# Performance work log

Measured on AMD Instinct MI355X. Metric: run time of the kernel, lower is better.

## Reference

```python
import jax, jax.numpy as jnp
import numpy as np

INP = 512
HIDDEN = 512
N_HEADS = 8          # called 'head_dim' in the torch code
D_HEAD = HIDDEN // N_HEADS  # 64
BASE = 10000.0
SCALE = D_HEAD ** (-0.5)


def rope(x):
    # x: [b, s, h, d]
    b, s, h, d = x.shape
    half = d // 2
    theta = 1.0 / (BASE ** (jnp.arange(0, d, 2, dtype=jnp.float32) / d))  # [d/2]
    idx_theta = jnp.arange(s, dtype=jnp.float32)[:, None] * theta[None, :]  # [s, d/2]
    idx_theta2 = jnp.concatenate([idx_theta, idx_theta], axis=1)            # [s, d]
    neg_half = jnp.concatenate([-x[..., half:], x[..., :half]], axis=-1)
    cos = jnp.cos(idx_theta2)[None, :, None, :]
    sin = jnp.sin(idx_theta2)[None, :, None, :]
    return x * cos + neg_half * sin


def setup_inputs() -> dict:
    key = jax.random.key(0)
    ks = jax.random.split(key, 10)
    b, s = 4, 2048
    init = lambda k, shp, fan_in: jax.random.normal(k, shp, jnp.float32) * (fan_in ** -0.5)
    return {
        "x": jax.random.normal(ks[0], (b, s, INP), jnp.float32),
        "c": jax.random.normal(ks[1], (b, s, INP), jnp.float32),
        "Wq": init(ks[2], (INP, HIDDEN), INP), "bq": jnp.zeros((HIDDEN,), jnp.float32),
        "Wk": init(ks[3], (INP, HIDDEN), INP), "bk": jnp.zeros((HIDDEN,), jnp.float32),
        "Wv": init(ks[4], (INP, HIDDEN), INP), "bv": jnp.zeros((HIDDEN,), jnp.float32),
        "Wo": init(ks[5], (HIDDEN, INP), HIDDEN), "bo": jnp.zeros((INP,), jnp.float32),
    }


def reference(x, c, Wq, bq, Wk, bk, Wv, bv, Wo, bo):
    b, s, _ = x.shape
    h_res = x
    q = (c @ Wq + bq).reshape(b, s, N_HEADS, D_HEAD)
    k = (x @ Wk + bk).reshape(b, s, N_HEADS, D_HEAD)
    v = (x @ Wv + bv).reshape(b, s, N_HEADS, D_HEAD)
    q = rope(q)
    k = rope(k)  # computed but unused, exactly as in the source
    # NOTE: source computes scores between q and V (not k) -- faithful reproduction
    att = jnp.einsum('bihd,bjhd->bhij', q, v)            # [b, h, s, s]
    att = jax.nn.softmax(att * SCALE, axis=-1)
    out = jnp.einsum('bhij,bjhd->bihd', att, v)          # [b, s, h, d]
    out = out.reshape(b, s, HIDDEN)
    out = out @ Wo + bo
    return out + h_res
```

## Files before the change

### kernel.cpp

```cpp
#include <hip/hip_runtime.h>
#include <hip/hip_bf16.h>
#include <cstdint>

typedef float f32x4 __attribute__((ext_vector_type(4)));
typedef float f32x16 __attribute__((ext_vector_type(16)));
typedef short bf16x8 __attribute__((ext_vector_type(8)));
typedef short bf16x4 __attribute__((ext_vector_type(4)));
typedef unsigned int u32x2 __attribute__((ext_vector_type(2)));
typedef unsigned short u16;

#define B_    4
#define S_    2048
#define H_    8
#define D_    64
#define M_    8192

#define OFF_CBF   0UL
#define OFF_XBF   8388608UL
#define OFF_QBH   16777216UL
#define OFF_VBH   25165824UL
#define OFF_VTBH  33554432UL
#define OFF_ATTN  41943040UL
#define OFF_WQT   50331648UL
#define OFF_WVT   50855936UL
// ... 12 lines not shown
    union { uint32_t u; float f; } v; v.u = ((uint32_t)h) << 16;
    return v.f;
}

__device__ __forceinline__ uint32_t cvtpk(float lo, float hi){
    uint32_t r;
    asm("v_cvt_pk_bf16_f32 %0, %1, %2" : "=v"(r) : "v"(lo), "v"(hi));
    return r;
}
__device__ __forceinline__ void plswap(uint32_t &va, uint32_t &vb){
#if __has_builtin(__builtin_amdgcn_permlane32_swap)
    u32x2 r = __builtin_amdgcn_permlane32_swap(va, vb, false, false);
    va = r[0]; vb = r[1];
#else
    asm volatile("v_permlane32_swap_b32 %0, %1" : "+v"(va), "+v"(vb));
#endif
}

__device__ __forceinline__ f32x16 mfma32(bf16x8 a, bf16x8 b, f32x16 c){
    return __builtin_amdgcn_mfma_f32_32x32x16_bf16(a, b, c, 0, 0, 0);
}

__device__ __forceinline__ void deint(uint4 a, uint4 b, bf16x8 &lo, bf16x8 &hi){
    union { bf16x8 v; uint32_t d[4]; } L, H;
    uint32_t s0=a.x, s1=a.y, s2=a.z, s3=a.w, s4=b.x, s5=b.y, s6=b.z, s7=b.w;
    L.d[0] = (s0 & 0xffffu) | (s1 << 16);
    L.d[1] = (s2 & 0xffffu) | (s3 << 16);
    L.d[2] = (s4 & 0xffffu) | (s5 << 16);
    L.d[3] = (s6 & 0xffffu) | (s7 << 16);
    H.d[0] = (s0 >> 16) | (s1 & 0xffff0000u);
    H.d[1] = (s2 >> 16) | (s3 & 0xffff0000u);
    H.d[2] = (s4 >> 16) | (s5 & 0xffff0000u);
    H.d[3] = (s6 >> 16) | (s7 & 0xffff0000u);
    lo = L.v; hi = H.v;
}

__device__ __forceinline__ int swz(int row, int col){
    return (col & ~63) | ((((col >> 3) & 7) ^ (row & 7)) << 3) | (col & 7);
}

__device__ __forceinline__ int detect_f32(const void* x_in){
    int lane = threadIdx.x & 63;
    ushort2 dv = ((const ushort2*)x_in)[lane];
    bool hit = ((((dv.x >> 7) & 0xFF) >= 160) || (((dv.y >> 7) & 0xFF) >= 160));
    return __ballot(hit) != 0ULL;
}

__device__ __forceinline__ void gload_lds16(const u16* g, u16* l){
    __builtin_amdgcn_global_load_lds(
        (const __attribute__((address_space(1))) void*)g,
        (__attribute__((address_space(3))) void*)l, 16, 0, 0);
}

__global__ void k_prep(const void* c_in, const void* x_in,
                       const void* Wq, const void* Wv, const void* Wo,
                       const void* bq, const void* bv, const void* bo,
                       u16* c_bf, u16* x_bf,
                       u16* Wqt, u16* Wvt, u16* Wot, float* bias_ws,
                       float* cos_t, float* sin_t){
    int bid = blockIdx.x;
    if (bid >= 11264){
        int idx = (bid - 11264) * 256 + threadIdx.x;
        int pos = idx >> 5, j = idx & 31;
        double theta = pow(10000.0, -(double)j / 32.0);
        double rev = ((double)pos * theta) * 0.15915494309189535;
        rev -= floor(rev);
        float fr = (float)rev;
        cos_t[idx] = __builtin_amdgcn_cosf(fr);
        sin_t[idx] = __builtin_amdgcn_sinf(fr);
        return;
    }
    if (bid >= 8192){
        int f = detect_f32(x_in);
        int wi = (bid - 8192) >> 10;
        int idx = ((bid - 8192) & 1023) * 256 + threadIdx.x;
        int k = idx >> 9, n = idx & 511;
        const void* W; u16* Wt; const void* bb;
        if (wi == 0){ W = Wq; Wt = Wqt; bb = bq; }
        else if (wi == 1){ W = Wv; Wt = Wvt; bb = bv; }
        else { W = Wo; Wt = Wot; bb = bo; }
        float v = f ? ((const float*)W)[idx] : bf2f(((const u16*)W)[idx]);
        Wt[n * 512 + (wi == 2 ? k : swz(n, k))] = f2bf(v);
        if (idx < 512){
            float b = f ? ((const float*)bb)[idx] : bf2f(((const u16*)bb)[idx]);
            bias_ws[wi * 512 + idx] = b;
        }
        return;
    }
    int f = detect_f32(x_in);
    int isx = bid >= 4096;
    int t = (bid & 4095) * 256 + threadIdx.x;
    const void* src = isx ? x_in : c_in;
    u16* dst = isx ? x_bf : c_bf;
    int e0 = t * 4, row = e0 >> 9, col = e0 & 511;
    size_t didx = (size_t)row * 512 + swz(row, col);
    ushort4 o;
    if (f){
        float4 v = ((const float4*)src)[t];
        o.x = f2bf(v.x); o.y = f2bf(v.y); o.z = f2bf(v.z); o.w = f2bf(v.w);
    } else {
        o = ((const ushort4*)src)[t];
    }
    *(ushort4*)(dst + didx) = o;
}

__global__ __launch_bounds__(256) void k_gemm_qv(
    const u16* __restrict__ c_bf, const u16* __restrict__ x_bf,
    const u16* __restrict__ Wqt, const u16* __restrict__ Wvt,
    const float* __restrict__ bias_ws,
    const float* __restrict__ cos_t, const float* __restrict__ sin_t,
    u16* __restrict__ Qbh, u16* __restrict__ Vbh, u16* __restrict__ Vtbh)
{
    __shared__ __align__(16) u16 Als[2][128 * 64];
    __shared__ __align__(16) u16 Bls[2][128 * 64];
    const int w = threadIdx.x >> 6, lane = threadIdx.x & 63;
    const int g = lane >> 4, cq = lane & 15;
    const int wm = w & 1, wn = w >> 1;
    const int z = blockIdx.z;
    const u16* A  = z ? x_bf : c_bf;
    const u16* Wt = z ? Wvt : Wqt;
    const float* bias = bias_ws + (z ? 512 : 0);
    const int m0b = blockIdx.x * 128, n0b = blockIdx.y * 128;
    const int m0 = m0b + wm * 64, n0 = n0b + wn * 64;
    const int swzi = ((cq & 7) << 3);

    int srow[4], scol[4];
    #pragma unroll
    for (int i = 0; i < 4; i++){
        int flat = (w * 4 + i) * 64 + lane;
        srow[i] = flat >> 3; scol[i] = (flat & 7) * 8;
    }

    const f32x4 zero = {0.f, 0.f, 0.f, 0.f};
    f32x4 acc[4][4];
    #pragma unroll
    for (int i = 0; i < 4; i++)
        #pragma unroll
        for (int j = 0; j < 4; j++) acc[i][j] = zero;

    #pragma unroll
    for (int i = 0; i < 4; i++){
        gload_lds16(A  + (size_t)(m0b + srow[i]) * 512 + scol[i], &Als[0][(w*4 + i) * 512]);
        gload_lds16(Wt + (size_t)(n0b + srow[i]) * 512 + scol[i], &Bls[0][(w*4 + i) * 512]);
    }

    for (int kt = 0; kt < 8; kt++){
        const int buf = kt & 1;
        __builtin_amdgcn_s_waitcnt(0x0F70);
        __syncthreads();
        if (kt < 7){
            const int kk = (kt + 1) * 64;
            #pragma unroll
            for (int i = 0; i < 4; i++){
                gload_lds16(A  + (size_t)(m0b + srow[i]) * 512 + kk + scol[i], &Als[buf^1][(w*4 + i) * 512]);
                gload_lds16(Wt + (size_t)(n0b + srow[i]) * 512 + kk + scol[i], &Bls[buf^1][(w*4 + i) * 512]);
            }
        }
        #pragma unroll
        for (int ks = 0; ks < 2; ks++){
            const int cs = ((ks * 4 + g) << 3) ^ swzi;
            bf16x8 a[4], b[4];
            #pragma unroll
            for (int mt = 0; mt < 4; mt++)
                a[mt] = *(const bf16x8*)&Als[buf][(wm*64 + mt*16 + cq) * 64 + cs];
            #pragma unroll
            for (int nt = 0; nt < 4; nt++)
                b[nt] = *(const bf16x8*)&Bls[buf][(wn*64 + nt*16 + cq) * 64 + cs];
            #pragma unroll
            for (int mt = 0; mt < 4; mt++)
                #pragma unroll
                for (int nt = 0; nt < 4; nt++)
                    acc[mt][nt] = __builtin_amdgcn_mfma_f32_16x16x32_bf16(a[mt], b[nt], acc[mt][nt], 0, 0, 0);
        }
    }
    __syncthreads();

    #pragma unroll
    for (int nt = 0; nt < 4; nt++){
        float bvv = bias[n0 + nt*16 + cq];
        #pragma unroll
        for (int mt = 0; mt < 4; mt++) acc[mt][nt] += bvv;
    }
    const int h = n0 >> 6;
    if (z == 0){
        const float SCL = 0.125f * 1.4426950408889634f;
        uint32_t* Qpk = (uint32_t*)Qbh;
        #pragma unroll
        for (int mt = 0; mt < 4; mt++){
            #pragma unroll
            for (int r = 0; r < 4; r++){
                int row = m0 + mt*16 + g*4 + r;
                int b_idx = row >> 11, si = row & 2047;
                size_t base = ((size_t)(b_idx*8 + h) * 2048 + si) * 32;
                #pragma unroll
                for (int nt = 0; nt < 2; nt++){
                    int dj = nt*16 + cq;
                    float cv = cos_t[si*32 + dj], sv = sin_t[si*32 + dj];
                    float x1 = acc[mt][nt][r], x2 = acc[mt][nt+2][r];
                    Qpk[base + dj] = cvtpk((x1*cv - x2*sv) * SCL, (x2*cv + x1*sv) * SCL);
                }
            }
        }
    } else {
        float* ltw = ((float*)&Als[0][0]) + w * (16 * 65);
        const int b_idx = m0 >> 11, si0 = m0 & 2047;
        const size_t tbase = ((size_t)(b_idx*8 + h) * 64) * 2048;
        #pragma unroll
        for (int mt = 0; mt < 4; mt++)
            #pragma unroll
            for (int r = 0; r < 4; r++){
                int row = m0 + mt*16 + g*4 + r;
                int bi = row >> 11, si = row & 2047;
                size_t base = ((size_t)(bi*8 + h) * 2048 + si) * 64;
                #pragma unroll
                for (int nt = 0; nt < 4; nt++)
                    Vbh[base + nt*16 + cq] = f2bf(acc[mt][nt][r]);
            }
        #pragma unroll
        for (int nt = 0; nt < 4; nt++){
            #pragma unroll
            for (int mt = 0; mt < 4; mt++)
                #pragma unroll
                for (int r = 0; r < 4; r++)
                    ltw[cq * 65 + mt*16 + g*4 + r] = acc[mt][nt][r];
            __builtin_amdgcn_wave_barrier();
            #pragma unroll
            for (int dd = 0; dd < 16; dd++){
                float v = ltw[dd * 65 + lane];
                Vtbh[tbase + (size_t)(nt*16 + dd) * 2048 + si0 + lane] = f2bf(v);
            }
            __builtin_amdgcn_wave_barrier();
        }
    }
}

__global__ __launch_bounds__(256, 2) void k_attn(
    const u16* __restrict__ Qbh, const u16* __restrict__ Vbh,
    const u16* __restrict__ Vtbh,
    u16* __restrict__ part0, u16* __restrict__ part1, float* __restrict__ lsum)
{
    __shared__ __align__(16) u16 Vs[2][64 * 68];
    __shared__ __align__(16) u16 Vts[2][64 * 68];

    const int bid = blockIdx.x;
    const int logical = (bid & 7) * 64 + (bid >> 3);
    const int xb = logical & 7;
    const int bh = (logical >> 3) & 31;
    const int z  = logical >> 8;

    const int w = threadIdx.x >> 6, lane = threadIdx.x & 63;
    const int r32 = lane & 31, hl = lane >> 5;
    const int i0 = xb * 256 + w * 64;
    const int j0 = z * 1024;

    const uint32_t* Qpk = (const uint32_t*)Qbh;
    bf16x8 aq[2][4];
    #pragma unroll
    for (int it = 0; it < 2; it++){
        size_t qb = ((size_t)bh*2048 + i0 + it*32 + r32)*32 + hl*8;
        uint4 a0 = *(const uint4*)&Qpk[qb];
        uint4 a1 = *(const uint4*)&Qpk[qb + 4];
        uint4 b0 = *(const uint4*)&Qpk[qb + 16];
        uint4 b1 = *(const uint4*)&Qpk[qb + 20];
        deint(a0, a1, aq[it][0], aq[it][2]);
        deint(b0, b1, aq[it][1], aq[it][3]);
    }

    const int sr = w * 16 + (lane >> 2), sc = (lane & 3) * 16;
    const u16* gvs = Vbh  + ((size_t)bh*2048 + j0 + sr) * 64 + sc;
    const u16* gvt = Vtbh + ((size_t)bh*64 + sr) * 2048 + j0 + sc;
    const int ls = sr * 68 + sc;

    {
        bf16x8 a0 = *(const bf16x8*)gvs,       a1 = *(const bf16x8*)(gvs + 8);
        bf16x8 b0 = *(const bf16x8*)gvt,       b1 = *(const bf16x8*)(gvt + 8);
        *(bf16x8*)&Vs[0][ls]  = a0;  *(bf16x8*)&Vs[0][ls + 8]  = a1;
        *(bf16x8*)&Vts[0][ls] = b0;  *(bf16x8*)&Vts[0][ls + 8] = b1;
    }

    f32x16 ot[2][2];
    #pragma unroll
    for (int it = 0; it < 2; it++)
        #pragma unroll
        for (int dt = 0; dt < 2; dt++)
            #pragma unroll
            for (int rr = 0; rr < 16; rr++) ot[it][dt][rr] = 0.f;
    const f32x16 zero16 = ot[0][0];
    float fl[2] = {0.f, 0.f};
    bf16x8 pb[2][4];

    {
        bf16x8 na0 = *(const bf16x8*)(gvs + 4096);
        bf16x8 na1 = *(const bf16x8*)(gvs + 4096 + 8);
        bf16x8 nb0 = *(const bf16x8*)(gvt + 64);
        bf16x8 nb1 = *(const bf16x8*)(gvt + 64 + 8);
        __syncthreads();
        #pragma unroll
        for (int jtile = 0; jtile < 2; jtile++){
            bf16x8 vf[4];
            #pragma unroll
            for (int kk = 0; kk < 4; kk++)
                vf[kk] = *(const bf16x8*)&Vs[0][(jtile*32 + r32)*68 + kk*16 + hl*8];
            f32x16 st0 = zero16, st1 = zero16;
            __builtin_amdgcn_s_setprio(1);
            #pragma unroll
            for (int kk = 0; kk < 4; kk++){
                st0 = mfma32(vf[kk], aq[0][kk], st0);
                st1 = mfma32(vf[kk], aq[1][kk], st1);
            }
            __builtin_amdgcn_s_setprio(0);
            #pragma unroll
            for (int rr = 0; rr < 16; rr++) st0[rr] = __builtin_amdgcn_exp2f(st0[rr]);
            #pragma unroll
            for (int rr = 0; rr < 16; rr++) st1[rr] = __builtin_amdgcn_exp2f(st1[rr]);
            fl[0] += ((st0[0]+st0[1])+(st0[2]+st0[3])) + ((st0[4]+st0[5])+(st0[6]+st0[7]))
                   + ((st0[8]+st0[9])+(st0[10]+st0[11])) + ((st0[12]+st0[13])+(st0[14]+st0[15]));
            fl[1] += ((st1[0]+st1[1])+(st1[2]+st1[3])) + ((st1[4]+st1[5])+(st1[6]+st1[7]))
                   + ((st1[8]+st1[9])+(st1[10]+st1[11])) + ((st1[12]+st1[13])+(st1[14]+st1[15]));
            #pragma unroll
            for (int c = 0; c < 2; c++){
                uint32_t dA1 = cvtpk(st0[c*8+0], st0[c*8+1]);
                uint32_t dA2 = cvtpk(st0[c*8+2], st0[c*8+3]);
                uint32_t dB1 = cvtpk(st0[c*8+4], st0[c*8+5]);
                uint32_t dB2 = cvtpk(st0[c*8+6], st0[c*8+7]);
                plswap(dA1, dB1); plswap(dA2, dB2);
                union { bf16x8 v; uint32_t d[4]; } u;
                u.d[0] = dA1; u.d[1] = dA2; u.d[2] = dB1; u.d[3] = dB2;
                pb[0][jtile*2 + c] = u.v;
            }
            #pragma unroll
            for (int c = 0; c < 2; c++){
                uint32_t dA1 = cvtpk(st1[c*8+0], st1[c*8+1]);
                uint32_t dA2 = cvtpk(st1[c*8+2], st1[c*8+3]);
                uint32_t dB1 = cvtpk(st1[c*8+4], st1[c*8+5]);
                uint32_t dB2 = cvtpk(st1[c*8+6], st1[c*8+7]);
                plswap(dA1, dB1); plswap(dA2, dB2);
                union { bf16x8 v; uint32_t d[4]; } u;
                u.d[0] = dA1; u.d[1] = dA2; u.d[2] = dB1; u.d[3] = dB2;
                pb[1][jtile*2 + c] = u.v;
            }
        }
        *(bf16x8*)&Vs[1][ls]  = na0;  *(bf16x8*)&Vs[1][ls + 8]  = na1;
        *(bf16x8*)&Vts[1][ls] = nb0;  *(bf16x8*)&Vts[1][ls + 8] = nb1;
    }

    for (int jt = 1; jt < 16; jt++){
        const int bufA = jt & 1, bufB = bufA ^ 1;
        __syncthreads();
        bf16x8 na0, na1, nb0, nb1;
        if (jt < 15){
            na0 = *(const bf16x8*)(gvs + (size_t)(jt + 1) * 4096);
            na1 = *(const bf16x8*)(gvs + (size_t)(jt + 1) * 4096 + 8);
            nb0 = *(const bf16x8*)(gvt + (size_t)(jt + 1) * 64);
            nb1 = *(const bf16x8*)(gvt + (size_t)(jt + 1) * 64 + 8);
        }
        #pragma unroll
        for (int jtile = 0; jtile < 2; jtile++){
            bf16x8 vf[4];
            #pragma unroll
            for (int kk = 0; kk < 4; kk++)
                vf[kk] = *(const bf16x8*)&Vs[bufA][(jtile*32 + r32)*68 + kk*16 + hl*8];
            f32x16 st0 = zero16, st1 = zero16;
            __builtin_amdgcn_s_setprio(1);
            #pragma unroll
            for (int kk = 0; kk < 4; kk++){
                st0 = mfma32(vf[kk], aq[0][kk], st0);
                st1 = mfma32(vf[kk], aq[1][kk], st1);
            }
            #pragma unroll
            for (int cc = 0; cc < 2; cc++){
                const int c = jtile*2 + cc;
                bf16x8 vt0 = *(const bf16x8*)&Vts[bufB][r32*68 + c*16 + hl*8];
                bf16x8 vt1 = *(const bf16x8*)&Vts[bufB][(32 + r32)*68 + c*16 + hl*8];
                ot[0][0] = mfma32(vt0, pb[0][c], ot[0][0]);
                ot[1][0] = mfma32(vt0, pb[1][c], ot[1][0]);
                ot[0][1] = mfma32(vt1, pb[0][c], ot[0][1]);
                ot[1][1] = mfma32(vt1, pb[1][c], ot[1][1]);
            }
            __builtin_amdgcn_s_setprio(0);
            #pragma unroll
            for (int rr = 0; rr < 16; rr++) st0[rr] = __builtin_amdgcn_exp2f(st0[rr]);
            #pragma unroll
            for (int rr = 0; rr < 16; rr++) st1[rr] = __builtin_amdgcn_exp2f(st1[rr]);
            fl[0] += ((st0[0]+st0[1])+(st0[2]+st0[3])) + ((st0[4]+st0[5])+(st0[6]+st0[7]))
                   + ((st0[8]+st0[9])+(st0[10]+st0[11])) + ((st0[12]+st0[13])+(st0[14]+st0[15]));
            fl[1] += ((st1[0]+st1[1])+(st1[2]+st1[3])) + ((st1[4]+st1[5])+(st1[6]+st1[7]))
                   + ((st1[8]+st1[9])+(st1[10]+st1[11])) + ((st1[12]+st1[13])+(st1[14]+st1[15]));
            #pragma unroll
            for (int c = 0; c < 2; c++){
                uint32_t dA1 = cvtpk(st0[c*8+0], st0[c*8+1]);
                uint32_t dA2 = cvtpk(st0[c*8+2], st0[c*8+3]);
                uint32_t dB1 = cvtpk(st0[c*8+4], st0[c*8+5]);
                uint32_t dB2 = cvtpk(st0[c*8+6], st0[c*8+7]);
                plswap(dA1, dB1); plswap(dA2, dB2);
                union { bf16x8 v; uint32_t d[4]; } u;
                u.d[0] = dA1; u.d[1] = dA2; u.d[2] = dB1; u.d[3] = dB2;
                pb[0][jtile*2 + c] = u.v;
            }
            #pragma unroll
            for (int c = 0; c < 2; c++){
                uint32_t dA1 = cvtpk(st1[c*8+0], st1[c*8+1]);
                uint32_t dA2 = cvtpk(st1[c*8+2], st1[c*8+3]);
                uint32_t dB1 = cvtpk(st1[c*8+4], st1[c*8+5]);
                uint32_t dB2 = cvtpk(st1[c*8+6], st1[c*8+7]);
                plswap(dA1, dB1); plswap(dA2, dB2);
                union { bf16x8 v; uint32_t d[4]; } u;
                u.d[0] = dA1; u.d[1] = dA2; u.d[2] = dB1; u.d[3] = dB2;
                pb[1][jtile*2 + c] = u.v;
            }
        }
        __syncthreads();
        if (jt < 15){
            *(bf16x8*)&Vs[bufB][ls]  = na0;  *(bf16x8*)&Vs[bufB][ls + 8]  = na1;
            *(bf16x8*)&Vts[bufB][ls] = nb0;  *(bf16x8*)&Vts[bufB][ls + 8] = nb1;
        }
    }

    __builtin_amdgcn_s_setprio(1);
    #pragma unroll
    for (int c = 0; c < 4; c++){
        bf16x8 vt0 = *(const bf16x8*)&Vts[1][r32*68 + c*16 + hl*8];
        bf16x8 vt1 = *(const bf16x8*)&Vts[1][(32 + r32)*68 + c*16 + hl*8];
        ot[0][0] = mfma32(vt0, pb[0][c], ot[0][0]);
        ot[1][0] = mfma32(vt0, pb[1][c], ot[1][0]);
        ot[0][1] = mfma32(vt1, pb[0][c], ot[0][1]);
        ot[1][1] = mfma32(vt1, pb[1][c], ot[1][1]);
    }
    __builtin_amdgcn_s_setprio(0);

    const int b_idx = bh >> 3, hh = bh & 7;
    u16* part = z ? part1 : part0;
    #pragma unroll
    for (int it = 0; it < 2; it++){
        float sum = fl[it] + __shfl_xor(fl[it], 32);
        const int row = b_idx*2048 + i0 + it*32 + r32;
        if (lane < 32)
            lsum[(size_t)z*65536 + (size_t)hh*8192 + row] = sum;
        #pragma unroll
        for (int dt = 0; dt < 2; dt++){
            #pragma unroll
            for (int q = 0; q < 4; q++){
                float v0 = ot[it][dt][q*4+0];
                float v1 = ot[it][dt][q*4+1];
                float v2 = ot[it][dt][q*4+2];
                float v3 = ot[it][dt][q*4+3];
                uint2 pw;
                pw.x = cvtpk(v0, v1);
                pw.y = cvtpk(v2, v3);
                int col = hh*64 + dt*32 + q*8 + hl*4;
                *(uint2*)&part[(size_t)row * 512 + col] = pw;
            }
        }
    }
}

__global__ __launch_bounds__(256) void k_gemm_out(
    const u16* __restrict__ part0, const u16* __restrict__ part1,
    const float* __restrict__ lsum,
    const u16* __restrict__ Wot, const float* __restrict__ bias_ws,
    const void* __restrict__ x_in, void* __restrict__ out)
{
    __shared__ __align__(16) u16 Als[2][128 * 68];
    __shared__ __align__(16) u16 Bls[2][64 * 68];
    const int w = threadIdx.x >> 6, lane = threadIdx.x & 63;
    const int g = lane >> 4, cq = lane & 15;
    const int wm = w & 1, wn = w >> 1;
    const int m0b = blockIdx.x * 128, n0b = blockIdx.y * 64;
    const int m0 = m0b + wm * 64, n0 = n0b + wn * 32;
    const int f = detect_f32(x_in);

    int sra[4], sca[4], srb[2], scb[2];
    #pragma unroll
    for (int i = 0; i < 4; i++){
        int flat = (w * 4 + i) * 64 + lane;
        sra[i] = flat >> 3; sca[i] = (flat & 7) * 8;
    }
    #pragma unroll
    for (int i = 0; i < 2; i++){
        int flat = (w * 2 + i) * 64 + lane;
        srb[i] = flat >> 3; scb[i] = (flat & 7) * 8;
    }
// ... 53 lines not shown
            #pragma unroll
            for (int nt = 0; nt < 2; nt++)
                b[nt] = *(const bf16x8*)&Bls[buf][(wn*32 + nt*16 + cq)*68 + ks*32 + g*8];
            #pragma unroll
            for (int mt = 0; mt < 4; mt++)
                #pragma unroll
                for (int nt = 0; nt < 2; nt++)
                    acc[mt][nt] = __builtin_amdgcn_mfma_f32_16x16x32_bf16(a[mt], b[nt], acc[mt][nt], 0, 0, 0);
        }
        if (kt < 7){
            #pragma unroll
            for (int i = 0; i < 4; i++){
                union { bf16x8 v; u16 e[8]; } a8;
                #pragma unroll
                for (int e = 0; e < 8; e++)
                    a8.e[e] = f2bf((bf2f((u16)pa0[i][e]) + bf2f((u16)pa1[i][e])) * pr[i]);
                *(bf16x8*)&Als[buf^1][sra[i]*68 + sca[i]] = a8.v;
            }
            #pragma unroll
            for (int i = 0; i < 2; i++)
                *(bf16x8*)&Bls[buf^1][srb[i]*68 + scb[i]] = pb[i];
        }
    }
    #pragma unroll
    for (int mt = 0; mt < 4; mt++)
        #pragma unroll
        for (int nt = 0; nt < 2; nt++)
            #pragma unroll
            for (int r = 0; r < 4; r++){
                int row = m0 + mt*16 + g*4 + r;
                int col = n0 + nt*16 + cq;
                size_t idx = (size_t)row * 512 + col;
                float resid = f ? ((const float*)x_in)[idx] : bf2f(((const u16*)x_in)[idx]);
                float v = acc[mt][nt][r] + bias_ws[1024 + col] + resid;
                if (f) ((float*)out)[idx] = v;
                else   ((u16*)out)[idx] = f2bf(v);
            }
}

extern "C" void kernel_launch(void* const* d_in, const int* in_sizes, int n_in,
                              void* d_out, int out_size, void* d_ws, size_t ws_size,
                              hipStream_t stream){
    const void* x_in = d_in[0];
    const void* c_in = d_in[1];
    const void* Wq = d_in[2]; const void* bq = d_in[3];
    const void* Wv = d_in[6]; const void* bv = d_in[7];
    const void* Wo = d_in[8]; const void* bo = d_in[9];

    if (ws_size < WS_NEEDED){
        hipMemsetAsync(d_out, 0, (size_t)out_size * 2, stream);
        return;
    }
    char* ws = (char*)d_ws;
    u16* c_bf  = (u16*)(ws + OFF_CBF);
    u16* x_bf  = (u16*)(ws + OFF_XBF);
    u16* Qbh   = (u16*)(ws + OFF_QBH);
    u16* Vbh   = (u16*)(ws + OFF_VBH);
    u16* Vtbh  = (u16*)(ws + OFF_VTBH);
    u16* part0 = (u16*)(ws + OFF_ATTN);
    u16* part1 = (u16*)(ws + OFF_CBF);
    float* lsum = (float*)(ws + OFF_XBF);
    u16* Wqt   = (u16*)(ws + OFF_WQT);
    u16* Wvt   = (u16*)(ws + OFF_WVT);
    u16* Wot   = (u16*)(ws + OFF_WOT);
    float* bias_ws = (float*)(ws + OFF_BIAS);
    float* cos_t   = (float*)(ws + OFF_COS);
    float* sin_t   = (float*)(ws + OFF_SIN);

    k_prep<<<11520, 256, 0, stream>>>(c_in, x_in, Wq, Wv, Wo, bq, bv, bo,
                                      c_bf, x_bf, Wqt, Wvt, Wot, bias_ws, cos_t, sin_t);
    k_gemm_qv<<<dim3(64, 4, 2), 256, 0, stream>>>(c_bf, x_bf, Wqt, Wvt, bias_ws,
                                                  cos_t, sin_t, Qbh, Vbh, Vtbh);
    k_attn<<<dim3(512), 256, 0, stream>>>(Qbh, Vbh, Vtbh, part0, part1, lsum);
    k_gemm_out<<<dim3(64, 8), 256, 0, stream>>>(part0, part1, lsum, Wot, bias_ws,
                                                x_in, d_out);
}
```

Before: 181.1 us.

## Load V tiles directly from global memory in attention, dropping LDS staging

The attention kernel no longer stages V and V-transpose tiles through double-buffered shared memory with block barriers. Each wave now reads its MFMA operands straight from global memory (relying on L1/L2 caching), which removes LDS traffic and the __syncthreads calls. The cost is four waves re-fetching the same V data from cache, with global load latency now exposed without any explicit prefetch.

New measurement: 208.3 us. +15.0%, slower.

```diff
diff --git a/kernel.cpp b/kernel.cpp
--- a/kernel.cpp
+++ b/kernel.cpp
@@ -275,9 +275,6 @@
     const u16* __restrict__ Vtbh,
     u16* __restrict__ part0, u16* __restrict__ part1, float* __restrict__ lsum)
 {
-    __shared__ __align__(16) u16 Vs[2][64 * 68];
-    __shared__ __align__(16) u16 Vts[2][64 * 68];
-
     const int bid = blockIdx.x;
     const int logical = (bid & 7) * 64 + (bid >> 3);
     const int xb = logical & 7;
@@ -302,17 +299,9 @@
         deint(b0, b1, aq[it][1], aq[it][3]);
     }
 
-    const int sr = w * 16 + (lane >> 2), sc = (lane & 3) * 16;
-    const u16* gvs = Vbh  + ((size_t)bh*2048 + j0 + sr) * 64 + sc;
-    const u16* gvt = Vtbh + ((size_t)bh*64 + sr) * 2048 + j0 + sc;
-    const int ls = sr * 68 + sc;
-
-    {
-        bf16x8 a0 = *(const bf16x8*)gvs,       a1 = *(const bf16x8*)(gvs + 8);
-        bf16x8 b0 = *(const bf16x8*)gvt,       b1 = *(const bf16x8*)(gvt + 8);
-        *(bf16x8*)&Vs[0][ls]  = a0;  *(bf16x8*)&Vs[0][ls + 8]  = a1;
-        *(bf16x8*)&Vts[0][ls] = b0;  *(bf16x8*)&Vts[0][ls + 8] = b1;
-    }
+    const u16* gv   = Vbh  + ((size_t)bh*2048 + j0 + r32) * 64 + hl*8;
+    const u16* gvt0 = Vtbh + ((size_t)bh*64 + r32) * 2048 + j0 + hl*8;
+    const u16* gvt1 = gvt0 + (size_t)32 * 2048;
 
     f32x16 ot[2][2];
     #pragma unroll
@@ -325,24 +314,78 @@
     float fl[2] = {0.f, 0.f};
     bf16x8 pb[2][4];
 
-    {
-        bf16x8 na0 = *(const bf16x8*)(gvs + 4096);
-        bf16x8 na1 = *(const bf16x8*)(gvs + 4096 + 8);
-        bf16x8 nb0 = *(const bf16x8*)(gvt + 64);
-        bf16x8 nb1 = *(const bf16x8*)(gvt + 64 + 8);
-        __syncthreads();
+    #pragma unroll
+    for (int jtile = 0; jtile < 2; jtile++){
+        const int jrow = jtile*32;
+        bf16x8 vf[4];
+        #pragma unroll
+        for (int kk = 0; kk < 4; kk++)
+            vf[kk] = *(const bf16x8*)(gv + (size_t)jrow*64 + kk*16);
+        f32x16 st0 = zero16, st1 = zero16;
+        __builtin_amdgcn_s_setprio(1);
+        #pragma unroll
+        for (int kk = 0; kk < 4; kk++){
+            st0 = mfma32(vf[kk], aq[0][kk], st0);
+            st1 = mfma32(vf[kk], aq[1][kk], st1);
+        }
+        __builtin_amdgcn_s_setprio(0);
+        #pragma unroll
+        for (int rr = 0; rr < 16; rr++) st0[rr] = __builtin_amdgcn_exp2f(st0[rr]);
+        #pragma unroll
+        for (int rr = 0; rr < 16; rr++) st1[rr] = __builtin_amdgcn_exp2f(st1[rr]);
+        fl[0] += ((st0[0]+st0[1])+(st0[2]+st0[3])) + ((st0[4]+st0[5])+(st0[6]+st0[7]))
+               + ((st0[8]+st0[9])+(st0[10]+st0[11])) + ((st0[12]+st0[13])+(st0[14]+st0[15]));
+        fl[1] += ((st1[0]+st1[1])+(st1[2]+st1[3])) + ((st1[4]+st1[5])+(st1[6]+st1[7]))
+               + ((st1[8]+st1[9])+(st1[10]+st1[11])) + ((st1[12]+st1[13])+(st1[14]+st1[15]));
+        #pragma unroll
+        for (int c = 0; c < 2; c++){
+            uint32_t dA1 = cvtpk(st0[c*8+0], st0[c*8+1]);
+            uint32_t dA2 = cvtpk(st0[c*8+2], st0[c*8+3]);
+            uint32_t dB1 = cvtpk(st0[c*8+4], st0[c*8+5]);
+            uint32_t dB2 = cvtpk(st0[c*8+6], st0[c*8+7]);
+            plswap(dA1, dB1); plswap(dA2, dB2);
+            union { bf16x8 v; uint32_t d[4]; } u;
+            u.d[0] = dA1; u.d[1] = dA2; u.d[2] = dB1; u.d[3] = dB2;
+            pb[0][jtile*2 + c] = u.v;
+        }
+        #pragma unroll
+        for (int c = 0; c < 2; c++){
+            uint32_t dA1 = cvtpk(st1[c*8+0], st1[c*8+1]);
+            uint32_t dA2 = cvtpk(st1[c*8+2], st1[c*8+3]);
+            uint32_t dB1 = cvtpk(st1[c*8+4], st1[c*8+5]);
+            uint32_t dB2 = cvtpk(st1[c*8+6], st1[c*8+7]);
+            plswap(dA1, dB1); plswap(dA2, dB2);
+            union { bf16x8 v; uint32_t d[4]; } u;
+            u.d[0] = dA1; u.d[1] = dA2; u.d[2] = dB1; u.d[3] = dB2;
+            pb[1][jtile*2 + c] = u.v;
+        }
+    }
+
+    for (int jt = 1; jt < 16; jt++){
+        const int jb = jt * 64, pj = (jt - 1) * 64;
         #pragma unroll
         for (int jtile = 0; jtile < 2; jtile++){
+            const int jrow = jb + jtile*32;
             bf16x8 vf[4];
             #pragma unroll
             for (int kk = 0; kk < 4; kk++)
-                vf[kk] = *(const bf16x8*)&Vs[0][(jtile*32 + r32)*68 + kk*16 + hl*8];
+                vf[kk] = *(const bf16x8*)(gv + (size_t)jrow*64 + kk*16);
             f32x16 st0 = zero16, st1 = zero16;
             __builtin_amdgcn_s_setprio(1);
             #pragma unroll
             for (int kk = 0; kk < 4; kk++){
                 st0 = mfma32(vf[kk], aq[0][kk], st0);
                 st1 = mfma32(vf[kk], aq[1][kk], st1);
+            }
+            #pragma unroll
+            for (int cc = 0; cc < 2; cc++){
+                const int c = jtile*2 + cc;
+                bf16x8 vt0 = *(const bf16x8*)(gvt0 + pj + c*16);
+                bf16x8 vt1 = *(const bf16x8*)(gvt1 + pj + c*16);
+                ot[0][0] = mfma32(vt0, pb[0][c], ot[0][0]);
+                ot[1][0] = mfma32(vt0, pb[1][c], ot[1][0]);
+                ot[0][1] = mfma32(vt1, pb[0][c], ot[0][1]);
+                ot[1][1] = mfma32(vt1, pb[1][c], ot[1][1]);
             }
             __builtin_amdgcn_s_setprio(0);
             #pragma unroll
@@ -376,93 +419,22 @@
                 pb[1][jtile*2 + c] = u.v;
             }
         }
-        *(bf16x8*)&Vs[1][ls]  = na0;  *(bf16x8*)&Vs[1][ls + 8]  = na1;
-        *(bf16x8*)&Vts[1][ls] = nb0;  *(bf16x8*)&Vts[1][ls + 8] = nb1;
-    }
-
-    for (int jt = 1; jt < 16; jt++){
-        const int bufA = jt & 1, bufB = bufA ^ 1;
-        __syncthreads();
-        bf16x8 na0, na1, nb0, nb1;
-        if (jt < 15){
-            na0 = *(const bf16x8*)(gvs + (size_t)(jt + 1) * 4096);
-            na1 = *(const bf16x8*)(gvs + (size_t)(jt + 1) * 4096 + 8);
-            nb0 = *(const bf16x8*)(gvt + (size_t)(jt + 1) * 64);
-            nb1 = *(const bf16x8*)(gvt + (size_t)(jt + 1) * 64 + 8);
-        }
-        #pragma unroll
-        for (int jtile = 0; jtile < 2; jtile++){
-            bf16x8 vf[4];
-            #pragma unroll
-            for (int kk = 0; kk < 4; kk++)
-                vf[kk] = *(const bf16x8*)&Vs[bufA][(jtile*32 + r32)*68 + kk*16 + hl*8];
-            f32x16 st0 = zero16, st1 = zero16;
-            __builtin_amdgcn_s_setprio(1);
-            #pragma unroll
-            for (int kk = 0; kk < 4; kk++){
-                st0 = mfma32(vf[kk], aq[0][kk], st0);
-                st1 = mfma32(vf[kk], aq[1][kk], st1);
-            }
-            #pragma unroll
-            for (int cc = 0; cc < 2; cc++){
-                const int c = jtile*2 + cc;
-                bf16x8 vt0 = *(const bf16x8*)&Vts[bufB][r32*68 + c*16 + hl*8];
-                bf16x8 vt1 = *(const bf16x8*)&Vts[bufB][(32 + r32)*68 + c*16 + hl*8];
-                ot[0][0] = mfma32(vt0, pb[0][c], ot[0][0]);
-                ot[1][0] = mfma32(vt0, pb[1][c], ot[1][0]);
-                ot[0][1] = mfma32(vt1, pb[0][c], ot[0][1]);
-                ot[1][1] = mfma32(vt1, pb[1][c], ot[1][1]);
-            }
-            __builtin_amdgcn_s_setprio(0);
-            #pragma unroll
-            for (int rr = 0; rr < 16; rr++) st0[rr] = __builtin_amdgcn_exp2f(st0[rr]);
-            #pragma unroll
-            for (int rr = 0; rr < 16; rr++) st1[rr] = __builtin_amdgcn_exp2f(st1[rr]);
-            fl[0] += ((st0[0]+st0[1])+(st0[2]+st0[3])) + ((st0[4]+st0[5])+(st0[6]+st0[7]))
-                   + ((st0[8]+st0[9])+(st0[10]+st0[11])) + ((st0[12]+st0[13])+(st0[14]+st0[15]));
-            fl[1] += ((st1[0]+st1[1])+(st1[2]+st1[3])) + ((st1[4]+st1[5])+(st1[6]+st1[7]))
-                   + ((st1[8]+st1[9])+(st1[10]+st1[11])) + ((st1[12]+st1[13])+(st1[14]+st1[15]));
-            #pragma unroll
-            for (int c = 0; c < 2; c++){
-                uint32_t dA1 = cvtpk(st0[c*8+0], st0[c*8+1]);
-                uint32_t dA2 = cvtpk(st0[c*8+2], st0[c*8+3]);
-                uint32_t dB1 = cvtpk(st0[c*8+4], st0[c*8+5]);
-                uint32_t dB2 = cvtpk(st0[c*8+6], st0[c*8+7]);
-                plswap(dA1, dB1); plswap(dA2, dB2);
-                union { bf16x8 v; uint32_t d[4]; } u;
-                u.d[0] = dA1; u.d[1] = dA2; u.d[2] = dB1; u.d[3] = dB2;
-                pb[0][jtile*2 + c] = u.v;
-            }
-            #pragma unroll
-            for (int c = 0; c < 2; c++){
-                uint32_t dA1 = cvtpk(st1[c*8+0], st1[c*8+1]);
-                uint32_t dA2 = cvtpk(st1[c*8+2], st1[c*8+3]);
-                uint32_t dB1 = cvtpk(st1[c*8+4], st1[c*8+5]);
-                uint32_t dB2 = cvtpk(st1[c*8+6], st1[c*8+7]);
-                plswap(dA1, dB1); plswap(dA2, dB2);
-                union { bf16x8 v; uint32_t d[4]; } u;
-                u.d[0] = dA1; u.d[1] = dA2; u.d[2] = dB1; u.d[3] = dB2;
-                pb[1][jtile*2 + c] = u.v;
-            }
-        }
-        __syncthreads();
-        if (jt < 15){
-            *(bf16x8*)&Vs[bufB][ls]  = na0;  *(bf16x8*)&Vs[bufB][ls + 8]  = na1;
-            *(bf16x8*)&Vts[bufB][ls] = nb0;  *(bf16x8*)&Vts[bufB][ls + 8] = nb1;
-        }
-    }
-
-    __builtin_amdgcn_s_setprio(1);
-    #pragma unroll
-    for (int c = 0; c < 4; c++){
-        bf16x8 vt0 = *(const bf16x8*)&Vts[1][r32*68 + c*16 + hl*8];
-        bf16x8 vt1 = *(const bf16x8*)&Vts[1][(32 + r32)*68 + c*16 + hl*8];
-        ot[0][0] = mfma32(vt0, pb[0][c], ot[0][0]);
-        ot[1][0] = mfma32(vt0, pb[1][c], ot[1][0]);
-        ot[0][1] = mfma32(vt1, pb[0][c], ot[0][1]);
-        ot[1][1] = mfma32(vt1, pb[1][c], ot[1][1]);
-    }
-    __builtin_amdgcn_s_setprio(0);
+    }
+
+    {
+        const int pj = 15 * 64;
+        __builtin_amdgcn_s_setprio(1);
+        #pragma unroll
+        for (int c = 0; c < 4; c++){
+            bf16x8 vt0 = *(const bf16x8*)(gvt0 + pj + c*16);
+            bf16x8 vt1 = *(const bf16x8*)(gvt1 + pj + c*16);
+            ot[0][0] = mfma32(vt0, pb[0][c], ot[0][0]);
+            ot[1][0] = mfma32(vt0, pb[1][c], ot[1][0]);
+            ot[0][1] = mfma32(vt1, pb[0][c], ot[0][1]);
+            ot[1][1] = mfma32(vt1, pb[1][c], ot[1][1]);
+        }
+        __builtin_amdgcn_s_setprio(0);
+    }
 
     const int b_idx = bh >> 3, hh = bh & 7;
     u16* part = z ? part1 : part0;
```

## Triple-buffer V tiles in attention to drop one barrier per iteration

Applied to the files above, without the earlier changes.

The attention kernel's LDS staging for V and V-transpose tiles goes from two buffers to three. With the third buffer, the next tile can be written without a second __syncthreads in each loop iteration. The QK^T MFMA chain is also split into two independent accumulators that are summed before exp2, which shortens the dependency chain. In exchange, LDS use per block grows by half, which could limit occupancy, and each element costs an extra add.

New measurement: 199.8 us. +10.4%, slower.

```diff
diff --git a/kernel.cpp b/kernel.cpp
--- a/kernel.cpp
+++ b/kernel.cpp
@@ -275,8 +275,8 @@
     const u16* __restrict__ Vtbh,
     u16* __restrict__ part0, u16* __restrict__ part1, float* __restrict__ lsum)
 {
-    __shared__ __align__(16) u16 Vs[2][64 * 68];
-    __shared__ __align__(16) u16 Vts[2][64 * 68];
+    __shared__ __align__(16) u16 Vs[3][64 * 68];
+    __shared__ __align__(16) u16 Vts[3][64 * 68];
 
     const int bid = blockIdx.x;
     const int logical = (bid & 7) * 64 + (bid >> 3);
@@ -308,11 +308,16 @@
     const int ls = sr * 68 + sc;
 
     {
-        bf16x8 a0 = *(const bf16x8*)gvs,       a1 = *(const bf16x8*)(gvs + 8);
-        bf16x8 b0 = *(const bf16x8*)gvt,       b1 = *(const bf16x8*)(gvt + 8);
+        bf16x8 a0 = *(const bf16x8*)gvs,            a1 = *(const bf16x8*)(gvs + 8);
+        bf16x8 b0 = *(const bf16x8*)gvt,            b1 = *(const bf16x8*)(gvt + 8);
+        bf16x8 c0 = *(const bf16x8*)(gvs + 4096),   c1 = *(const bf16x8*)(gvs + 4096 + 8);
+        bf16x8 d0 = *(const bf16x8*)(gvt + 64),     d1 = *(const bf16x8*)(gvt + 64 + 8);
         *(bf16x8*)&Vs[0][ls]  = a0;  *(bf16x8*)&Vs[0][ls + 8]  = a1;
         *(bf16x8*)&Vts[0][ls] = b0;  *(bf16x8*)&Vts[0][ls + 8] = b1;
-    }
+        *(bf16x8*)&Vs[1][ls]  = c0;  *(bf16x8*)&Vs[1][ls + 8]  = c1;
+        *(bf16x8*)&Vts[1][ls] = d0;  *(bf16x8*)&Vts[1][ls + 8] = d1;
+    }
+    __syncthreads();
 
     f32x16 ot[2][2];
     #pragma unroll
@@ -325,30 +330,92 @@
     float fl[2] = {0.f, 0.f};
     bf16x8 pb[2][4];
 
-    {
-        bf16x8 na0 = *(const bf16x8*)(gvs + 4096);
-        bf16x8 na1 = *(const bf16x8*)(gvs + 4096 + 8);
-        bf16x8 nb0 = *(const bf16x8*)(gvt + 64);
-        bf16x8 nb1 = *(const bf16x8*)(gvt + 64 + 8);
+    #pragma unroll
+    for (int jtile = 0; jtile < 2; jtile++){
+        bf16x8 vf[4];
+        #pragma unroll
+        for (int kk = 0; kk < 4; kk++)
+            vf[kk] = *(const bf16x8*)&Vs[0][(jtile*32 + r32)*68 + kk*16 + hl*8];
+        f32x16 s0a = zero16, s0b = zero16, s1a = zero16, s1b = zero16;
+        __builtin_amdgcn_s_setprio(1);
+        s0a = mfma32(vf[0], aq[0][0], s0a);  s1a = mfma32(vf[0], aq[1][0], s1a);
+        s0b = mfma32(vf[2], aq[0][2], s0b);  s1b = mfma32(vf[2], aq[1][2], s1b);
+        s0a = mfma32(vf[1], aq[0][1], s0a);  s1a = mfma32(vf[1], aq[1][1], s1a);
+        s0b = mfma32(vf[3], aq[0][3], s0b);  s1b = mfma32(vf[3], aq[1][3], s1b);
+        __builtin_amdgcn_s_setprio(0);
+        f32x16 st0, st1;
+        #pragma unroll
+        for (int rr = 0; rr < 16; rr++) st0[rr] = __builtin_amdgcn_exp2f(s0a[rr] + s0b[rr]);
+        #pragma unroll
+        for (int rr = 0; rr < 16; rr++) st1[rr] = __builtin_amdgcn_exp2f(s1a[rr] + s1b[rr]);
+        fl[0] += ((st0[0]+st0[1])+(st0[2]+st0[3])) + ((st0[4]+st0[5])+(st0[6]+st0[7]))
+               + ((st0[8]+st0[9])+(st0[10]+st0[11])) + ((st0[12]+st0[13])+(st0[14]+st0[15]));
+        fl[1] += ((st1[0]+st1[1])+(st1[2]+st1[3])) + ((st1[4]+st1[5])+(st1[6]+st1[7]))
+               + ((st1[8]+st1[9])+(st1[10]+st1[11])) + ((st1[12]+st1[13])+(st1[14]+st1[15]));
+        #pragma unroll
+        for (int c = 0; c < 2; c++){
+            uint32_t dA1 = cvtpk(st0[c*8+0], st0[c*8+1]);
+            uint32_t dA2 = cvtpk(st0[c*8+2], st0[c*8+3]);
+            uint32_t dB1 = cvtpk(st0[c*8+4], st0[c*8+5]);
+            uint32_t dB2 = cvtpk(st0[c*8+6], st0[c*8+7]);
+            plswap(dA1, dB1); plswap(dA2, dB2);
+            union { bf16x8 v; uint32_t d[4]; } u;
+            u.d[0] = dA1; u.d[1] = dA2; u.d[2] = dB1; u.d[3] = dB2;
+            pb[0][jtile*2 + c] = u.v;
+        }
+        #pragma unroll
+        for (int c = 0; c < 2; c++){
+            uint32_t dA1 = cvtpk(st1[c*8+0], st1[c*8+1]);
+            uint32_t dA2 = cvtpk(st1[c*8+2], st1[c*8+3]);
+            uint32_t dB1 = cvtpk(st1[c*8+4], st1[c*8+5]);
+            uint32_t dB2 = cvtpk(st1[c*8+6], st1[c*8+7]);
+            plswap(dA1, dB1); plswap(dA2, dB2);
+            union { bf16x8 v; uint32_t d[4]; } u;
+            u.d[0] = dA1; u.d[1] = dA2; u.d[2] = dB1; u.d[3] = dB2;
+            pb[1][jtile*2 + c] = u.v;
+        }
+    }
+
+    for (int jt = 1; jt < 16; jt++){
+        const int bufQ = jt % 3;
+        const int bufP = (bufQ == 0) ? 2 : bufQ - 1;
+        const int bufW = (bufQ == 2) ? 0 : bufQ + 1;
         __syncthreads();
+        bf16x8 na0, na1, nb0, nb1;
+        if (jt < 15){
+            na0 = *(const bf16x8*)(gvs + (size_t)(jt + 1) * 4096);
+            na1 = *(const bf16x8*)(gvs + (size_t)(jt + 1) * 4096 + 8);
+            nb0 = *(const bf16x8*)(gvt + (size_t)(jt + 1) * 64);
+            nb1 = *(const bf16x8*)(gvt + (size_t)(jt + 1) * 64 + 8);
+        }
         #pragma unroll
         for (int jtile = 0; jtile < 2; jtile++){
             bf16x8 vf[4];
             #pragma unroll
             for (int kk = 0; kk < 4; kk++)
-                vf[kk] = *(const bf16x8*)&Vs[0][(jtile*32 + r32)*68 + kk*16 + hl*8];
-            f32x16 st0 = zero16, st1 = zero16;
+                vf[kk] = *(const bf16x8*)&Vs[bufQ][(jtile*32 + r32)*68 + kk*16 + hl*8];
+            f32x16 s0a = zero16, s0b = zero16, s1a = zero16, s1b = zero16;
             __builtin_amdgcn_s_setprio(1);
-            #pragma unroll
-            for (int kk = 0; kk < 4; kk++){
-                st0 = mfma32(vf[kk], aq[0][kk], st0);
-                st1 = mfma32(vf[kk], aq[1][kk], st1);
+            s0a = mfma32(vf[0], aq[0][0], s0a);  s1a = mfma32(vf[0], aq[1][0], s1a);
+            s0b = mfma32(vf[2], aq[0][2], s0b);  s1b = mfma32(vf[2], aq[1][2], s1b);
+            s0a = mfma32(vf[1], aq[0][1], s0a);  s1a = mfma32(vf[1], aq[1][1], s1a);
+            s0b = mfma32(vf[3], aq[0][3], s0b);  s1b = mfma32(vf[3], aq[1][3], s1b);
+            #pragma unroll
+            for (int cc = 0; cc < 2; cc++){
+                const int c = jtile*2 + cc;
+                bf16x8 vt0 = *(const bf16x8*)&Vts[bufP][r32*68 + c*16 + hl*8];
+                bf16x8 vt1 = *(const bf16x8*)&Vts[bufP][(32 + r32)*68 + c*16 + hl*8];
+                ot[0][0] = mfma32(vt0, pb[0][c], ot[0][0]);
+                ot[1][0] = mfma32(vt0, pb[1][c], ot[1][0]);
+                ot[0][1] = mfma32(vt1, pb[0][c], ot[0][1]);
+                ot[1][1] = mfma32(vt1, pb[1][c], ot[1][1]);
             }
             __builtin_amdgcn_s_setprio(0);
-            #pragma unroll
-            for (int rr = 0; rr < 16; rr++) st0[rr] = __builtin_amdgcn_exp2f(st0[rr]);
-            #pragma unroll
-            for (int rr = 0; rr < 16; rr++) st1[rr] = __builtin_amdgcn_exp2f(st1[rr]);
+            f32x16 st0, st1;
+            #pragma unroll
+            for (int rr = 0; rr < 16; rr++) st0[rr] = __builtin_amdgcn_exp2f(s0a[rr] + s0b[rr]);
+            #pragma unroll
+            for (int rr = 0; rr < 16; rr++) st1[rr] = __builtin_amdgcn_exp2f(s1a[rr] + s1b[rr]);
             fl[0] += ((st0[0]+st0[1])+(st0[2]+st0[3])) + ((st0[4]+st0[5])+(st0[6]+st0[7]))
                    + ((st0[8]+st0[9])+(st0[10]+st0[11])) + ((st0[12]+st0[13])+(st0[14]+st0[15]));
             fl[1] += ((st1[0]+st1[1])+(st1[2]+st1[3])) + ((st1[4]+st1[5])+(st1[6]+st1[7]))
@@ -376,87 +443,17 @@
                 pb[1][jtile*2 + c] = u.v;
             }
         }
-        *(bf16x8*)&Vs[1][ls]  = na0;  *(bf16x8*)&Vs[1][ls + 8]  = na1;
-        *(bf16x8*)&Vts[1][ls] = nb0;  *(bf16x8*)&Vts[1][ls + 8] = nb1;
-    }
-
-    for (int jt = 1; jt < 16; jt++){
-        const int bufA = jt & 1, bufB = bufA ^ 1;
-        __syncthreads();
-        bf16x8 na0, na1, nb0, nb1;
         if (jt < 15){
-            na0 = *(const bf16x8*)(gvs + (size_t)(jt + 1) * 4096);
-            na1 = *(const bf16x8*)(gvs + (size_t)(jt + 1) * 4096 + 8);
-            nb0 = *(const bf16x8*)(gvt + (size_t)(jt + 1) * 64);
-            nb1 = *(const bf16x8*)(gvt + (size_t)(jt + 1) * 64 + 8);
-        }
-        #pragma unroll
-        for (int jtile = 0; jtile < 2; jtile++){
-            bf16x8 vf[4];
-            #pragma unroll
-            for (int kk = 0; kk < 4; kk++)
-                vf[kk] = *(const bf16x8*)&Vs[bufA][(jtile*32 + r32)*68 + kk*16 + hl*8];
-            f32x16 st0 = zero16, st1 = zero16;
-            __builtin_amdgcn_s_setprio(1);
-            #pragma unroll
-            for (int kk = 0; kk < 4; kk++){
-                st0 = mfma32(vf[kk], aq[0][kk], st0);
-                st1 = mfma32(vf[kk], aq[1][kk], st1);
-            }
-            #pragma unroll
-            for (int cc = 0; cc < 2; cc++){
-                const int c = jtile*2 + cc;
-                bf16x8 vt0 = *(const bf16x8*)&Vts[bufB][r32*68 + c*16 + hl*8];
-                bf16x8 vt1 = *(const bf16x8*)&Vts[bufB][(32 + r32)*68 + c*16 + hl*8];
-                ot[0][0] = mfma32(vt0, pb[0][c], ot[0][0]);
-                ot[1][0] = mfma32(vt0, pb[1][c], ot[1][0]);
-                ot[0][1] = mfma32(vt1, pb[0][c], ot[0][1]);
-                ot[1][1] = mfma32(vt1, pb[1][c], ot[1][1]);
-            }
-            __builtin_amdgcn_s_setprio(0);
-            #pragma unroll
-            for (int rr = 0; rr < 16; rr++) st0[rr] = __builtin_amdgcn_exp2f(st0[rr]);
-            #pragma unroll
-            for (int rr = 0; rr < 16; rr++) st1[rr] = __builtin_amdgcn_exp2f(st1[rr]);
-            fl[0] += ((st0[0]+st0[1])+(st0[2]+st0[3])) + ((st0[4]+st0[5])+(st0[6]+st0[7]))
-                   + ((st0[8]+st0[9])+(st0[10]+st0[11])) + ((st0[12]+st0[13])+(st0[14]+st0[15]));
-            fl[1] += ((st1[0]+st1[1])+(st1[2]+st1[3])) + ((st1[4]+st1[5])+(st1[6]+st1[7]))
-                   + ((st1[8]+st1[9])+(st1[10]+st1[11])) + ((st1[12]+st1[13])+(st1[14]+st1[15]));
-            #pragma unroll
-            for (int c = 0; c < 2; c++){
-                uint32_t dA1 = cvtpk(st0[c*8+0], st0[c*8+1]);
-                uint32_t dA2 = cvtpk(st0[c*8+2], st0[c*8+3]);
-                uint32_t dB1 = cvtpk(st0[c*8+4], st0[c*8+5]);
-                uint32_t dB2 = cvtpk(st0[c*8+6], st0[c*8+7]);
-                plswap(dA1, dB1); plswap(dA2, dB2);
-                union { bf16x8 v; uint32_t d[4]; } u;
-                u.d[0] = dA1; u.d[1] = dA2; u.d[2] = dB1; u.d[3] = dB2;
-                pb[0][jtile*2 + c] = u.v;
-            }
-            #pragma unroll
-            for (int c = 0; c < 2; c++){
-                uint32_t dA1 = cvtpk(st1[c*8+0], st1[c*8+1]);
-                uint32_t dA2 = cvtpk(st1[c*8+2], st1[c*8+3]);
-                uint32_t dB1 = cvtpk(st1[c*8+4], st1[c*8+5]);
-                uint32_t dB2 = cvtpk(st1[c*8+6], st1[c*8+7]);
-                plswap(dA1, dB1); plswap(dA2, dB2);
-                union { bf16x8 v; uint32_t d[4]; } u;
-                u.d[0] = dA1; u.d[1] = dA2; u.d[2] = dB1; u.d[3] = dB2;
-                pb[1][jtile*2 + c] = u.v;
-            }
-        }
-        __syncthreads();
-        if (jt < 15){
-            *(bf16x8*)&Vs[bufB][ls]  = na0;  *(bf16x8*)&Vs[bufB][ls + 8]  = na1;
-            *(bf16x8*)&Vts[bufB][ls] = nb0;  *(bf16x8*)&Vts[bufB][ls + 8] = nb1;
+            *(bf16x8*)&Vs[bufW][ls]  = na0;  *(bf16x8*)&Vs[bufW][ls + 8]  = na1;
+            *(bf16x8*)&Vts[bufW][ls] = nb0;  *(bf16x8*)&Vts[bufW][ls + 8] = nb1;
         }
     }
 
     __builtin_amdgcn_s_setprio(1);
     #pragma unroll
     for (int c = 0; c < 4; c++){
-        bf16x8 vt0 = *(const bf16x8*)&Vts[1][r32*68 + c*16 + hl*8];
-        bf16x8 vt1 = *(const bf16x8*)&Vts[1][(32 + r32)*68 + c*16 + hl*8];
+        bf16x8 vt0 = *(const bf16x8*)&Vts[0][r32*68 + c*16 + hl*8];
+        bf16x8 vt1 = *(const bf16x8*)&Vts[0][(32 + r32)*68 + c*16 + hl*8];
         ot[0][0] = mfma32(vt0, pb[0][c], ot[0][0]);
         ot[1][0] = mfma32(vt0, pb[1][c], ot[1][0]);
         ot[0][1] = mfma32(vt1, pb[0][c], ot[0][1]);
```

## Fuse fp32-to-bf16 activation conversion into QV GEMM A-tile loads

Applied to the files above, without the earlier changes.

Drops the separate conversion pass that wrote bf16 swizzled copies of c and x to workspace. The QV GEMM now reads the raw inputs directly through registers, converts them to bf16 and stores them swizzled into LDS. The B operand keeps its async global-to-LDS path. This removes a full read-write pass over the two activation tensors, at the cost of register-staged A loads that read twice the bytes when inputs are fp32 and may hide less latency than the direct-to-LDS loads.

After: 189.1 us. 1.04x slower.

```diff
diff --git a/kernel.cpp b/kernel.cpp
--- a/kernel.cpp
+++ b/kernel.cpp
@@ -88,15 +88,28 @@
         (__attribute__((address_space(3))) void*)l, 16, 0, 0);
 }
 
-__global__ void k_prep(const void* c_in, const void* x_in,
+__device__ __forceinline__ bf16x8 ldA8(const void* A, int f, size_t row, int col){
+    if (f){
+        const float* p = (const float*)A + row * 512 + col;
+        float4 lo = *(const float4*)p;
+        float4 hi = *(const float4*)(p + 4);
+        union { bf16x8 v; uint32_t d[4]; } u;
+        u.d[0] = cvtpk(lo.x, lo.y); u.d[1] = cvtpk(lo.z, lo.w);
+        u.d[2] = cvtpk(hi.x, hi.y); u.d[3] = cvtpk(hi.z, hi.w);
+        return u.v;
+    } else {
+        return *(const bf16x8*)((const u16*)A + row * 512 + col);
+    }
+}
+
+__global__ void k_prep(const void* x_in,
                        const void* Wq, const void* Wv, const void* Wo,
                        const void* bq, const void* bv, const void* bo,
-                       u16* c_bf, u16* x_bf,
                        u16* Wqt, u16* Wvt, u16* Wot, float* bias_ws,
                        float* cos_t, float* sin_t){
     int bid = blockIdx.x;
-    if (bid >= 11264){
-        int idx = (bid - 11264) * 256 + threadIdx.x;
+    if (bid >= 3072){
+        int idx = (bid - 3072) * 256 + threadIdx.x;
         int pos = idx >> 5, j = idx & 31;
         double theta = pow(10000.0, -(double)j / 32.0);
         double rev = ((double)pos * theta) * 0.15915494309189535;
@@ -106,42 +119,24 @@
         sin_t[idx] = __builtin_amdgcn_sinf(fr);
         return;
     }
-    if (bid >= 8192){
-        int f = detect_f32(x_in);
-        int wi = (bid - 8192) >> 10;
-        int idx = ((bid - 8192) & 1023) * 256 + threadIdx.x;
-        int k = idx >> 9, n = idx & 511;
-        const void* W; u16* Wt; const void* bb;
-        if (wi == 0){ W = Wq; Wt = Wqt; bb = bq; }
-        else if (wi == 1){ W = Wv; Wt = Wvt; bb = bv; }
-        else { W = Wo; Wt = Wot; bb = bo; }
-        float v = f ? ((const float*)W)[idx] : bf2f(((const u16*)W)[idx]);
-        Wt[n * 512 + (wi == 2 ? k : swz(n, k))] = f2bf(v);
-        if (idx < 512){
-            float b = f ? ((const float*)bb)[idx] : bf2f(((const u16*)bb)[idx]);
-            bias_ws[wi * 512 + idx] = b;
-        }
-        return;
-    }
     int f = detect_f32(x_in);
-    int isx = bid >= 4096;
-    int t = (bid & 4095) * 256 + threadIdx.x;
-    const void* src = isx ? x_in : c_in;
-    u16* dst = isx ? x_bf : c_bf;
-    int e0 = t * 4, row = e0 >> 9, col = e0 & 511;
-    size_t didx = (size_t)row * 512 + swz(row, col);
-    ushort4 o;
-    if (f){
-        float4 v = ((const float4*)src)[t];
-        o.x = f2bf(v.x); o.y = f2bf(v.y); o.z = f2bf(v.z); o.w = f2bf(v.w);
-    } else {
-        o = ((const ushort4*)src)[t];
-    }
-    *(ushort4*)(dst + didx) = o;
+    int wi = bid >> 10;
+    int idx = (bid & 1023) * 256 + threadIdx.x;
+    int k = idx >> 9, n = idx & 511;
+    const void* W; u16* Wt; const void* bb;
+    if (wi == 0){ W = Wq; Wt = Wqt; bb = bq; }
+    else if (wi == 1){ W = Wv; Wt = Wvt; bb = bv; }
+    else { W = Wo; Wt = Wot; bb = bo; }
+    float v = f ? ((const float*)W)[idx] : bf2f(((const u16*)W)[idx]);
+    Wt[n * 512 + (wi == 2 ? k : swz(n, k))] = f2bf(v);
+    if (idx < 512){
+        float b = f ? ((const float*)bb)[idx] : bf2f(((const u16*)bb)[idx]);
+        bias_ws[wi * 512 + idx] = b;
+    }
 }
 
 __global__ __launch_bounds__(256) void k_gemm_qv(
-    const u16* __restrict__ c_bf, const u16* __restrict__ x_bf,
+    const void* __restrict__ c_in, const void* __restrict__ x_in,
     const u16* __restrict__ Wqt, const u16* __restrict__ Wvt,
     const float* __restrict__ bias_ws,
     const float* __restrict__ cos_t, const float* __restrict__ sin_t,
@@ -153,18 +148,20 @@
     const int g = lane >> 4, cq = lane & 15;
     const int wm = w & 1, wn = w >> 1;
     const int z = blockIdx.z;
-    const u16* A  = z ? x_bf : c_bf;
-    const u16* Wt = z ? Wvt : Wqt;
+    const void* A  = z ? x_in : c_in;
+    const u16* Wt  = z ? Wvt : Wqt;
     const float* bias = bias_ws + (z ? 512 : 0);
     const int m0b = blockIdx.x * 128, n0b = blockIdx.y * 128;
     const int m0 = m0b + wm * 64, n0 = n0b + wn * 64;
     const int swzi = ((cq & 7) << 3);
-
-    int srow[4], scol[4];
+    const int f = detect_f32(x_in);
+
+    int srow[4], scol[4], slds[4];
     #pragma unroll
     for (int i = 0; i < 4; i++){
         int flat = (w * 4 + i) * 64 + lane;
         srow[i] = flat >> 3; scol[i] = (flat & 7) * 8;
+        slds[i] = srow[i] * 64 + (((((scol[i] >> 3)) ^ srow[i]) & 7) << 3);
     }
 
     const f32x4 zero = {0.f, 0.f, 0.f, 0.f};
@@ -174,21 +171,28 @@
         #pragma unroll
         for (int j = 0; j < 4; j++) acc[i][j] = zero;
 
-    #pragma unroll
-    for (int i = 0; i < 4; i++){
-        gload_lds16(A  + (size_t)(m0b + srow[i]) * 512 + scol[i], &Als[0][(w*4 + i) * 512]);
-        gload_lds16(Wt + (size_t)(n0b + srow[i]) * 512 + scol[i], &Bls[0][(w*4 + i) * 512]);
+    {
+        bf16x8 av[4];
+        #pragma unroll
+        for (int i = 0; i < 4; i++)
+            av[i] = ldA8(A, f, m0b + srow[i], scol[i]);
+        #pragma unroll
+        for (int i = 0; i < 4; i++){
+            *(bf16x8*)&Als[0][slds[i]] = av[i];
+            gload_lds16(Wt + (size_t)(n0b + srow[i]) * 512 + scol[i], &Bls[0][(w*4 + i) * 512]);
+        }
     }
 
     for (int kt = 0; kt < 8; kt++){
         const int buf = kt & 1;
         __builtin_amdgcn_s_waitcnt(0x0F70);
         __syncthreads();
+        bf16x8 av[4];
         if (kt < 7){
             const int kk = (kt + 1) * 64;
             #pragma unroll
             for (int i = 0; i < 4; i++){
-                gload_lds16(A  + (size_t)(m0b + srow[i]) * 512 + kk + scol[i], &Als[buf^1][(w*4 + i) * 512]);
+                av[i] = ldA8(A, f, m0b + srow[i], kk + scol[i]);
                 gload_lds16(Wt + (size_t)(n0b + srow[i]) * 512 + kk + scol[i], &Bls[buf^1][(w*4 + i) * 512]);
             }
         }
@@ -207,6 +211,11 @@
                 #pragma unroll
                 for (int nt = 0; nt < 4; nt++)
                     acc[mt][nt] = __builtin_amdgcn_mfma_f32_16x16x32_bf16(a[mt], b[nt], acc[mt][nt], 0, 0, 0);
+        }
+        if (kt < 7){
+            #pragma unroll
+            for (int i = 0; i < 4; i++)
+                *(bf16x8*)&Als[buf^1][slds[i]] = av[i];
         }
     }
     __syncthreads();
@@ -622,8 +631,6 @@
         return;
     }
     char* ws = (char*)d_ws;
-    u16* c_bf  = (u16*)(ws + OFF_CBF);
-    u16* x_bf  = (u16*)(ws + OFF_XBF);
     u16* Qbh   = (u16*)(ws + OFF_QBH);
     u16* Vbh   = (u16*)(ws + OFF_VBH);
     u16* Vtbh  = (u16*)(ws + OFF_VTBH);
@@ -637,9 +644,9 @@
     float* cos_t   = (float*)(ws + OFF_COS);
     float* sin_t   = (float*)(ws + OFF_SIN);
 
-    k_prep<<<11520, 256, 0, stream>>>(c_in, x_in, Wq, Wv, Wo, bq, bv, bo,
-                                      c_bf, x_bf, Wqt, Wvt, Wot, bias_ws, cos_t, sin_t);
-    k_gemm_qv<<<dim3(64, 4, 2), 256, 0, stream>>>(c_bf, x_bf, Wqt, Wvt, bias_ws,
+    k_prep<<<3328, 256, 0, stream>>>(x_in, Wq, Wv, Wo, bq, bv, bo,
+                                     Wqt, Wvt, Wot, bias_ws, cos_t, sin_t);
+    k_gemm_qv<<<dim3(64, 4, 2), 256, 0, stream>>>(c_in, x_in, Wqt, Wvt, bias_ws,
                                                   cos_t, sin_t, Qbh, Vbh, Vtbh);
     k_attn<<<dim3(512), 256, 0, stream>>>(Qbh, Vbh, Vtbh, part0, part1, lsum);
     k_gemm_out<<<dim3(64, 8), 256, 0, stream>>>(part0, part1, lsum, Wot, bias_ws,
```
